# Kernel optimization log

Measured on AMD Instinct MI355X. Metric: run time of the kernel, lower is better.

## Reference

```python
import jax, jax.numpy as jnp
import numpy as np


def setup_inputs() -> dict:
    key = jax.random.key(0)
    k1, k2, k3 = jax.random.split(key, 3)
    B, S, D, R = 4, 4096, 2048, 8
    x = jax.random.normal(k1, (B, S, D), dtype=jnp.float32)
    # Linear weights stored as [out, in] like nn.Linear; module is .half()'d -> fp16
    Wq = (jax.random.normal(k2, (R, D), dtype=jnp.float32) * (D ** -0.5)).astype(jnp.float16)
    Wk = (jax.random.normal(k3, (R, D), dtype=jnp.float32) * (D ** -0.5)).astype(jnp.float16)
    return {"x": x, "Wq": Wq, "Wk": Wk}


def reference(x, Wq, Wk):
    # fp32 input is cast to fp16 (module calls x.half())
    xh = x.astype(jnp.float16)
    q = jnp.einsum('bsd,rd->bsr', xh, Wq)          # [B,S,8] fp16
    k = jnp.einsum('bsd,rd->bsr', xh, Wk)          # [B,S,8] fp16
    dots = jnp.einsum('btr,bsr->bts', q, k)        # [B,S,S] fp16
    scores = jax.nn.relu(dots)
    return scores.astype(jnp.float32)              # fp16 -> fp32 cast at end
```

## Files before the change

### kernel.cpp

```cpp
#include <hip/hip_runtime.h>

#define B_ 4
#define S_ 4096
#define D_ 2048
#define M_ (B_ * S_)
#define CHUNK 512
#define XSTR 520

typedef _Float16 v8h __attribute__((ext_vector_type(8)));
typedef _Float16 v4h __attribute__((ext_vector_type(4)));
typedef _Float16 v2h __attribute__((ext_vector_type(2)));
typedef float    v4f __attribute__((ext_vector_type(4)));

__global__ __launch_bounds__(256) void qk_proj_kernel(
    const float* __restrict__ x,
    const float* __restrict__ Wq,
    const float* __restrict__ Wk,
    unsigned short* __restrict__ q_ws,
    unsigned short* __restrict__ k_ws)
{
    __shared__ __align__(16) _Float16 xs[2][16 * XSTR];

    const int tid  = threadIdx.x;
    const int wave = tid >> 6;
    const int lane = tid & 63;
    const int quad = lane >> 4;
    const int col  = lane & 15;
    const int mbase = blockIdx.x * 16;

    const int srow = tid >> 7;
    const int sc4  = tid & 127;

    const float* wrow = (col < 8) ? (Wq + (size_t)col * D_)
                                  : (Wk + (size_t)(col - 8) * D_);

    float4 cur[8];
#pragma unroll
    for (int i = 0; i < 8; ++i) {
        const int row = i * 2 + srow;
        cur[i] = *(const float4*)(x + (size_t)(mbase + row) * D_ + sc4 * 4);
    }
#pragma unroll
    for (int i = 0; i < 8; ++i) {
        const int row = i * 2 + srow;
        v4h p = { (_Float16)cur[i].x, (_Float16)cur[i].y,
                  (_Float16)cur[i].z, (_Float16)cur[i].w };
        *(v4h*)&xs[0][row * XSTR + sc4 * 4] = p;
    }
    __syncthreads();

    v4f acc = {0.f, 0.f, 0.f, 0.f};

    for (int c = 0; c < 4; ++c) {
        float4 nxt[8];
        if (c < 3) {
#pragma unroll
            for (int i = 0; i < 8; ++i) {
                const int row = i * 2 + srow;
                nxt[i] = *(const float4*)(x + (size_t)(mbase + row) * D_
                                          + (c + 1) * CHUNK + sc4 * 4);
            }
        }
        const _Float16* xbuf = xs[c & 1];
#pragma unroll
        for (int s = 0; s < 4; ++s) {
            const int kloc = wave * 128 + s * 32 + quad * 8;
            v8h a = *(const v8h*)(xbuf + col * XSTR + kloc);
            const int kg = c * CHUNK + kloc;
            float4 w0 = *(const float4*)(wrow + kg);
            float4 w1 = *(const float4*)(wrow + kg + 4);
            v8h b;
            b[0]=(_Float16)w0.x; b[1]=(_Float16)w0.y;
            b[2]=(_Float16)w0.z; b[3]=(_Float16)w0.w;
            b[4]=(_Float16)w1.x; b[5]=(_Float16)w1.y;
            b[6]=(_Float16)w1.z; b[7]=(_Float16)w1.w;
            acc = __builtin_amdgcn_mfma_f32_16x16x32_f16(a, b, acc, 0, 0, 0);
        }
        if (c < 3) {
            _Float16* dbuf = xs[(c + 1) & 1];
#pragma unroll
            for (int i = 0; i < 8; ++i) {
                const int row = i * 2 + srow;
                v4h p = { (_Float16)nxt[i].x, (_Float16)nxt[i].y,
                          (_Float16)nxt[i].z, (_Float16)nxt[i].w };
                *(v4h*)&dbuf[row * XSTR + sc4 * 4] = p;
            }
            __syncthreads();
        }
    }

    __syncthreads();
    v4f* red = (v4f*)&xs[0][0];
    if (wave > 0) red[(wave - 1) * 64 + lane] = acc;
    __syncthreads();
    if (wave == 0) {
#pragma unroll
        for (int w = 0; w < 3; ++w) acc += red[w * 64 + lane];
#pragma unroll
        for (int reg = 0; reg < 4; ++reg) {
            const int row = mbase + quad * 4 + reg;
            const unsigned short h =
                __builtin_bit_cast(unsigned short, (_Float16)acc[reg]);
            if (col < 8) q_ws[(size_t)row * 8 + col] = h;
            else         k_ws[(size_t)row * 8 + (col - 8)] = h;
        }
    }
}

__global__ __launch_bounds__(256) void scores_kernel(
    const unsigned short* __restrict__ q_ws,
    const unsigned short* __restrict__ k_ws,
    float* __restrict__ out)
{
    __shared__ unsigned short kt[2048 * 8];
    __shared__ unsigned short qsh[16 * 8];

    const int tid   = threadIdx.x;
    const int tbase = blockIdx.x * 16;
    const int sbase = blockIdx.y * 2048;
    const int b     = blockIdx.z;

    {
        const uint4* src = (const uint4*)(k_ws + ((size_t)b * S_ + sbase) * 8);
        uint4* dst = (uint4*)kt;
#pragma unroll
        for (int i = 0; i < 8; ++i) dst[i * 256 + tid] = src[i * 256 + tid];
    }
    if (tid < 16) {
        ((uint4*)qsh)[tid] =
            *(const uint4*)(q_ws + ((size_t)b * S_ + tbase + tid) * 8);
    }
    __syncthreads();

    float* obase = out + ((size_t)b * S_ + tbase) * (size_t)S_ + sbase;

    for (int tl = 0; tl < 16; ++tl) {
        const uint4 qv = *(const uint4*)(qsh + tl * 8);
        const v2h q0 = __builtin_bit_cast(v2h, qv.x);
        const v2h q1 = __builtin_bit_cast(v2h, qv.y);
        const v2h q2 = __builtin_bit_cast(v2h, qv.z);
        const v2h q3 = __builtin_bit_cast(v2h, qv.w);
        float* orow = obase + (size_t)tl * S_;
#pragma unroll
        for (int ch = 0; ch < 8; ++ch) {
            const int s = ch * 256 + tid;
            const uint4 kv = *(const uint4*)(kt + s * 8);
#if __has_builtin(__builtin_amdgcn_fdot2)
            float d = 0.f;
            d = __builtin_amdgcn_fdot2(q0, __builtin_bit_cast(v2h, kv.x), d, false);
            d = __builtin_amdgcn_fdot2(q1, __builtin_bit_cast(v2h, kv.y), d, false);
            d = __builtin_amdgcn_fdot2(q2, __builtin_bit_cast(v2h, kv.z), d, false);
            d = __builtin_amdgcn_fdot2(q3, __builtin_bit_cast(v2h, kv.w), d, false);
#else
            const v2h ka = __builtin_bit_cast(v2h, kv.x);
            const v2h kb = __builtin_bit_cast(v2h, kv.y);
            const v2h kc = __builtin_bit_cast(v2h, kv.z);
            const v2h kd = __builtin_bit_cast(v2h, kv.w);
            float d = (float)q0[0]*(float)ka[0] + (float)q0[1]*(float)ka[1]
                    + (float)q1[0]*(float)kb[0] + (float)q1[1]*(float)kb[1]
                    + (float)q2[0]*(float)kc[0] + (float)q2[1]*(float)kc[1]
                    + (float)q3[0]*(float)kd[0] + (float)q3[1]*(float)kd[1];
#endif
            const float hv = (float)(_Float16)d;
            __builtin_nontemporal_store(hv > 0.f ? hv : 0.f, orow + s);
        }
    }
}

extern "C" void kernel_launch(void* const* d_in, const int* in_sizes, int n_in,
                              void* d_out, int out_size, void* d_ws, size_t ws_size,
                              hipStream_t stream) {
    const float* x  = (const float*)d_in[0];
    const float* Wq = (const float*)d_in[1];
    const float* Wk = (const float*)d_in[2];
    float* out = (float*)d_out;

    unsigned short* q_ws = (unsigned short*)d_ws;
    unsigned short* k_ws = q_ws + (size_t)M_ * 8;

    qk_proj_kernel<<<dim3(M_ / 16), dim3(256), 0, stream>>>(x, Wq, Wk, q_ws, k_ws);
    scores_kernel<<<dim3(S_ / 16, 2, B_), dim3(256), 0, stream>>>(q_ws, k_ws, out);
}
```

Before: 367.8 us.

## Hold K rows in registers and write 16-byte vectorized output stores in scores kernel

The scores kernel no longer stages a 2048-row K tile in shared memory. Each thread now loads four K rows straight from global memory into registers and reuses them across all 16 query rows. Each thread writes four consecutive fp32 outputs with one 128-bit nontemporal store instead of scalar stores. This removes the 32KB LDS staging and the LDS reads, which should raise occupancy and cut store instruction count for this write-bound kernel. In exchange, K loads are strided 64-byte chunks per thread and register pressure goes up.

```diff
diff --git a/kernel.cpp b/kernel.cpp
--- a/kernel.cpp
+++ b/kernel.cpp
@@ -107,12 +107,44 @@
     }
 }
 
+__device__ __forceinline__ float dot8(const uint4 qv, const uint4 kv) {
+#if __has_builtin(__builtin_amdgcn_fdot2)
+    float d = 0.f;
+    d = __builtin_amdgcn_fdot2(__builtin_bit_cast(v2h, qv.x),
+                               __builtin_bit_cast(v2h, kv.x), d, false);
+    d = __builtin_amdgcn_fdot2(__builtin_bit_cast(v2h, qv.y),
+                               __builtin_bit_cast(v2h, kv.y), d, false);
+    d = __builtin_amdgcn_fdot2(__builtin_bit_cast(v2h, qv.z),
+                               __builtin_bit_cast(v2h, kv.z), d, false);
+    d = __builtin_amdgcn_fdot2(__builtin_bit_cast(v2h, qv.w),
+                               __builtin_bit_cast(v2h, kv.w), d, false);
+    return d;
+#else
+    const v2h q0 = __builtin_bit_cast(v2h, qv.x);
+    const v2h q1 = __builtin_bit_cast(v2h, qv.y);
+    const v2h q2 = __builtin_bit_cast(v2h, qv.z);
+    const v2h q3 = __builtin_bit_cast(v2h, qv.w);
+    const v2h ka = __builtin_bit_cast(v2h, kv.x);
+    const v2h kb = __builtin_bit_cast(v2h, kv.y);
+    const v2h kc = __builtin_bit_cast(v2h, kv.z);
+    const v2h kd = __builtin_bit_cast(v2h, kv.w);
+    return (float)q0[0]*(float)ka[0] + (float)q0[1]*(float)ka[1]
+         + (float)q1[0]*(float)kb[0] + (float)q1[1]*(float)kb[1]
+         + (float)q2[0]*(float)kc[0] + (float)q2[1]*(float)kc[1]
+         + (float)q3[0]*(float)kd[0] + (float)q3[1]*(float)kd[1];
+#endif
+}
+
+__device__ __forceinline__ float relu_h(float d) {
+    const float hv = (float)(_Float16)d;
+    return hv > 0.f ? hv : 0.f;
+}
+
 __global__ __launch_bounds__(256) void scores_kernel(
     const unsigned short* __restrict__ q_ws,
     const unsigned short* __restrict__ k_ws,
     float* __restrict__ out)
 {
-    __shared__ unsigned short kt[2048 * 8];
     __shared__ unsigned short qsh[16 * 8];
 
     const int tid   = threadIdx.x;
@@ -120,12 +152,6 @@
     const int sbase = blockIdx.y * 2048;
     const int b     = blockIdx.z;
 
-    {
-        const uint4* src = (const uint4*)(k_ws + ((size_t)b * S_ + sbase) * 8);
-        uint4* dst = (uint4*)kt;
-#pragma unroll
-        for (int i = 0; i < 8; ++i) dst[i * 256 + tid] = src[i * 256 + tid];
-    }
     if (tid < 16) {
         ((uint4*)qsh)[tid] =
             *(const uint4*)(q_ws + ((size_t)b * S_ + tbase + tid) * 8);
@@ -134,35 +160,26 @@
 
     float* obase = out + ((size_t)b * S_ + tbase) * (size_t)S_ + sbase;
 
-    for (int tl = 0; tl < 16; ++tl) {
-        const uint4 qv = *(const uint4*)(qsh + tl * 8);
-        const v2h q0 = __builtin_bit_cast(v2h, qv.x);
-        const v2h q1 = __builtin_bit_cast(v2h, qv.y);
-        const v2h q2 = __builtin_bit_cast(v2h, qv.z);
-        const v2h q3 = __builtin_bit_cast(v2h, qv.w);
-        float* orow = obase + (size_t)tl * S_;
-#pragma unroll
-        for (int ch = 0; ch < 8; ++ch) {
-            const int s = ch * 256 + tid;
-            const uint4 kv = *(const uint4*)(kt + s * 8);
-#if __has_builtin(__builtin_amdgcn_fdot2)
-            float d = 0.f;
-            d = __builtin_amdgcn_fdot2(q0, __builtin_bit_cast(v2h, kv.x), d, false);
-            d = __builtin_amdgcn_fdot2(q1, __builtin_bit_cast(v2h, kv.y), d, false);
-            d = __builtin_amdgcn_fdot2(q2, __builtin_bit_cast(v2h, kv.z), d, false);
-            d = __builtin_amdgcn_fdot2(q3, __builtin_bit_cast(v2h, kv.w), d, false);
-#else
-            const v2h ka = __builtin_bit_cast(v2h, kv.x);
-            const v2h kb = __builtin_bit_cast(v2h, kv.y);
-            const v2h kc = __builtin_bit_cast(v2h, kv.z);
-            const v2h kd = __builtin_bit_cast(v2h, kv.w);
-            float d = (float)q0[0]*(float)ka[0] + (float)q0[1]*(float)ka[1]
-                    + (float)q1[0]*(float)kb[0] + (float)q1[1]*(float)kb[1]
-                    + (float)q2[0]*(float)kc[0] + (float)q2[1]*(float)kc[1]
-                    + (float)q3[0]*(float)kd[0] + (float)q3[1]*(float)kd[1];
-#endif
-            const float hv = (float)(_Float16)d;
-            __builtin_nontemporal_store(hv > 0.f ? hv : 0.f, orow + s);
+#pragma unroll
+    for (int ch = 0; ch < 2; ++ch) {
+        const int s0 = ch * 1024 + tid * 4;
+        const uint4* ksrc =
+            (const uint4*)(k_ws + ((size_t)b * S_ + sbase + s0) * 8);
+        const uint4 k0 = ksrc[0];
+        const uint4 k1 = ksrc[1];
+        const uint4 k2 = ksrc[2];
+        const uint4 k3 = ksrc[3];
+        float* ocol = obase + s0;
+
+#pragma unroll 4
+        for (int tl = 0; tl < 16; ++tl) {
+            const uint4 qv = *(const uint4*)(qsh + tl * 8);
+            v4f r;
+            r.x = relu_h(dot8(qv, k0));
+            r.y = relu_h(dot8(qv, k1));
+            r.z = relu_h(dot8(qv, k2));
+            r.w = relu_h(dot8(qv, k3));
+            __builtin_nontemporal_store(r, (v4f*)(ocol + (size_t)tl * S_));
         }
     }
 }
```

New measurement: 363.3 us. Within noise of the previous version (-1.2%).
